# Kernel tuning notes

Measured on AMD Instinct MI355X. Metric: run time of the kernel, lower is better.

Reference implementation:

```python
import jax, jax.numpy as jnp
from jax import lax
import numpy as np

H = 256      # encoder_hidden
F = 256      # variance predictor filter_size
K = 3        # kernel_size
NBINS = 256  # variance_embedding n_bins
B, S, T = 64, 512, 2048


def conv1d(x, w, b, pad):
    # x: [B, L, Cin], w: [K, Cin, Cout] -> [B, L, Cout]
    y = lax.conv_general_dilated(x, w, window_strides=(1,), padding=[(pad, pad)],
                                 dimension_numbers=('NWC', 'WIO', 'NWC'))
    return y + b


def layer_norm(x, g, b, eps=1e-5):
    mu = jnp.mean(x, -1, keepdims=True)
    v = jnp.mean((x - mu) ** 2, -1, keepdims=True)
    return (x - mu) * lax.rsqrt(v + eps) * g + b


def predictor(x, mask, w1, b1, g1, be1, w2, b2, g2, be2, lw, lb):
    h = jax.nn.relu(conv1d(x, w1, b1, (K - 1) // 2))
    h = layer_norm(h, g1, be1)
    h = jax.nn.relu(conv1d(h, w2, b2, 1))  # padding=1 hardcoded in original conv1d_2
    h = layer_norm(h, g2, be2)
    out = (h @ lw + lb)[..., 0]            # [B, L]
    return jnp.where(mask, 0.0, out)       # masked_fill(mask, 0.0)


def setup_inputs():
    key = jax.random.key(0)
    ks = jax.random.split(key, 16)
    inp = {
        'x': jax.random.normal(ks[0], (B, S, H), jnp.float32),
        'pitch_target': jax.random.normal(ks[1], (B, S), jnp.float32),
        'energy_target': jax.random.normal(ks[2], (B, S), jnp.float32),
        'src_mask': jnp.zeros((B, S), bool),
        'duration': jax.random.randint(ks[3], (B, S), 0, 4, jnp.int32),
        'max_len': T,
    }
    i = 4
    for p in ['d', 'p', 'e']:
        inp[p + '_w1'] = jax.random.normal(ks[i], (K, H, F), jnp.float32) * 0.05; i += 1
        inp[p + '_b1'] = jnp.zeros((F,), jnp.float32)
        inp[p + '_g1'] = jnp.ones((F,), jnp.float32)
        inp[p + '_be1'] = jnp.zeros((F,), jnp.float32)
        inp[p + '_w2'] = jax.random.normal(ks[i], (K, F, F), jnp.float32) * 0.05; i += 1
        inp[p + '_b2'] = jnp.zeros((F,), jnp.float32)
        inp[p + '_g2'] = jnp.ones((F,), jnp.float32)
        inp[p + '_be2'] = jnp.zeros((F,), jnp.float32)
        inp[p + '_lw'] = jax.random.normal(ks[i], (F, 1), jnp.float32) * 0.05; i += 1
        inp[p + '_lb'] = jnp.zeros((1,), jnp.float32)
    inp['p_table'] = jax.random.normal(ks[i], (NBINS, H), jnp.float32) * 0.02; i += 1
    inp['e_table'] = jax.random.normal(ks[i], (NBINS, H), jnp.float32) * 0.02
    return inp


def reference(x, pitch_target, energy_target, src_mask, duration, max_len,
              d_w1, d_b1, d_g1, d_be1, d_w2, d_b2, d_g2, d_be2, d_lw, d_lb,
              p_w1, p_b1, p_g1, p_be1, p_w2, p_b2, p_g2, p_be2, p_lw, p_lb,
              e_w1, e_b1, e_g1, e_be1, e_w2, e_b2, e_g2, e_be2, e_lw, e_lb,
              p_table, e_table):
    # linear-quantized bins over the data range (stats.json min/max -> [-2, 2] for randn data)
    bins = jnp.linspace(-2.0, 2.0, NBINS - 1, dtype=jnp.float32)

    log_d_pred = predictor(x, src_mask, d_w1, d_b1, d_g1, d_be1, d_w2, d_b2, d_g2, d_be2, d_lw, d_lb)

    # phoneme-level pitch (training path: target given -> embed bucketized target)
    p_pred = predictor(x, src_mask, p_w1, p_b1, p_g1, p_be1, p_w2, p_b2, p_g2, p_be2, p_lw, p_lb)
    p_emb = p_table[jnp.searchsorted(bins, pitch_target, side='left')]  # torch.bucketize(right=False)
    x = x + p_emb

    # phoneme-level energy (predictor runs on x AFTER pitch embedding, as in original)
    e_pred = predictor(x, src_mask, e_w1, e_b1, e_g1, e_be1, e_w2, e_b2, e_g2, e_be2, e_lw, e_lb)
    e_emb = e_table[jnp.searchsorted(bins, energy_target, side='left')]
    x = x + e_emb

    # Length regulation: expand phoneme i duration[b, i] times, pad to max_len.
    cum = jnp.cumsum(duration, axis=1)                 # [B, S]
    mel_len = cum[:, -1]                               # [B]
    frames = jnp.arange(max_len)                       # [T]
    # frame t maps to first phoneme i with cum[i] > t
    idx = jax.vmap(lambda c: jnp.searchsorted(c, frames, side='right'))(cum)  # [B, T]
    idx = jnp.minimum(idx, duration.shape[1] - 1)
    mel = jnp.take_along_axis(x, idx[:, :, None], axis=1)                     # [B, T, H]
    valid = frames[None, :] < mel_len[:, None]
    mel = jnp.where(valid[:, :, None], mel, 0.0)       # zero-pad beyond mel_len

    d_rounded = duration
    return (mel, p_pred, e_pred, log_d_pred, d_rounded, mel_len)
```

## Files before the change

kernel.cpp:

```cpp
#include <hip/hip_runtime.h>
#include <cstdint>
#include <cstddef>


#define HH 256
#define SS 512
#define BB 64
#define TT 2048

typedef __bf16 bf16;
typedef __attribute__((ext_vector_type(8))) __bf16 bf16x8;
typedef __attribute__((ext_vector_type(4))) __bf16 bf16x4;
typedef __attribute__((ext_vector_type(4))) float f32x4;

static constexpr size_t WSZ  = (size_t)3 * HH * HH;
static constexpr size_t H1SZ = (size_t)BB * SS * HH;

__device__ __forceinline__ int swz(int r, int c) { return (r * HH + c) ^ ((r & 7) << 3); }

__device__ __forceinline__ void gload16(const void* g, void* l) {
    __builtin_amdgcn_global_load_lds(
        (const __attribute__((address_space(1))) unsigned int*)g,
        (__attribute__((address_space(3))) unsigned int*)l, 16, 0, 0);
}

__device__ __forceinline__ float edge_val(int j) {
    const float step = 4.0f / 254.0f;
    if (j == 254) return 2.0f;
    return __fadd_rn(-2.0f, __fmul_rn((float)j, step));
}
__device__ __forceinline__ int bucket256(float v) {
    int lo = 0, hi = 255;
    while (lo < hi) {
        int mid = (lo + hi) >> 1;
        if (edge_val(mid) < v) lo = mid + 1; else hi = mid;
    }
    return lo;
}

__global__ void wt_pack(const float* __restrict__ w0, const float* __restrict__ w1,
                        const float* __restrict__ w2, const float* __restrict__ w3,
                        const float* __restrict__ w4, const float* __restrict__ w5,
                        bf16* __restrict__ wp) {
    const int cv = blockIdx.x / 3, k = blockIdx.x % 3;
    const float* wsel[6] = {w0, w1, w2, w3, w4, w5};
    const float* wk = wsel[cv] + (size_t)k * HH * HH;
    bf16* o = wp + ((size_t)(cv * 3 + k)) * HH * HH;
    for (int fb = 0; fb < 16; ++fb) {
        #pragma unroll
        for (int h = 0; h < 2; ++h) {
            const int idx  = threadIdx.x + 256 * h;
            const int kcb  = idx >> 6, lane = idx & 63;
            const int f    = fb * 16 + (lane & 15);
            const int c0   = kcb * 32 + (lane >> 4) * 8;
            bf16x8 v;
            #pragma unroll
            for (int j = 0; j < 8; ++j) v[j] = (bf16)wk[(size_t)(c0 + j) * HH + f];
            *(bf16x8*)(o + (((size_t)fb * 8 + kcb) * 64 + lane) * 8) = v;
        }
    }
}

__global__ __launch_bounds__(256) void xcvt_kernel(
    const float* __restrict__ x, const float* __restrict__ pt,
    const float* __restrict__ ptab,
    bf16* __restrict__ x1, bf16* __restrict__ x2)
{
    const int row = blockIdx.x * 8 + (threadIdx.x >> 5);
    const int c   = (threadIdx.x & 31) * 8;
    const int pb  = bucket256(pt[row]);
    const float4 v0 = *(const float4*)(x + (size_t)row * HH + c);
    const float4 v1 = *(const float4*)(x + (size_t)row * HH + c + 4);
    const float4 t0 = *(const float4*)(ptab + (size_t)pb * HH + c);
    const float4 t1 = *(const float4*)(ptab + (size_t)pb * HH + c + 4);
    bf16x8 a, b2;
    a[0] = (bf16)v0.x; a[1] = (bf16)v0.y; a[2] = (bf16)v0.z; a[3] = (bf16)v0.w;
    a[4] = (bf16)v1.x; a[5] = (bf16)v1.y; a[6] = (bf16)v1.z; a[7] = (bf16)v1.w;
    b2[0] = (bf16)(v0.x + t0.x); b2[1] = (bf16)(v0.y + t0.y);
    b2[2] = (bf16)(v0.z + t0.z); b2[3] = (bf16)(v0.w + t0.w);
    b2[4] = (bf16)(v1.x + t1.x); b2[5] = (bf16)(v1.y + t1.y);
    b2[6] = (bf16)(v1.z + t1.z); b2[7] = (bf16)(v1.w + t1.w);
    *(bf16x8*)(x1 + (size_t)row * HH + c) = a;
    *(bf16x8*)(x2 + (size_t)row * HH + c) = b2;
}

struct Args3 {
    const float* bias[3];
    const float* g[3];
    const float* be[3];
    const float* lw[3];
    const float* lb[3];
    float*       out[3];
};

__global__ __launch_bounds__(256, 3) void conv_fused(
    const bf16* __restrict__ x1,
    const bf16* __restrict__ x2,
    const bf16* __restrict__ wpk,
    Args3 a1, Args3 a2,
    const uint8_t* __restrict__ mask)
{
    __shared__ alignas(16) bf16 tile[84 * HH];
    __shared__ float red_s[80][4], red_q[80][4];
    __shared__ float ln_m[80], ln_r[80];

    const int tid    = threadIdx.x;
    const int pred   = blockIdx.x >> 9;
    const int within = blockIdx.x & 511;
    const int b      = within >> 3;
    const int s0     = (within & 7) * 64;

    const int lane = tid & 63;
    const int wv   = tid >> 6;

    const bf16* inb = (pred == 2 ? x2 : x1) + (size_t)b * SS * HH;
    const bf16* wt1 = wpk + (size_t)(pred * 2) * WSZ;
    const bf16* wt2 = wt1 + WSZ;

    for (int c = wv; c < 42; c += 4) {
        const int rrow = 2 * c + (lane >> 5);
        const int s    = s0 - 9 + rrow;
        const int sc   = min(max(s, 0), SS - 1);
        const char* src = (const char*)inb + (size_t)sc * 512
                        + (((lane & 31) * 16) ^ ((rrow & 7) << 4));
        gload16(src, (char*)tile + (size_t)c * 1024);
    }
    __syncthreads();
    if (s0 == 0) {
        for (int idx = tid; idx < 9 * 32; idx += 256) {
            const int r = idx >> 5, o = idx & 31;
            ((uint4*)tile)[r * 32 + o] = make_uint4(0u, 0u, 0u, 0u);
        }
    }
    if (s0 == SS - 64) {
        for (int idx = tid; idx < 11 * 32; idx += 256) {
            const int r = 73 + (idx >> 5), o = idx & 31;
            ((uint4*)tile)[r * 32 + o] = make_uint4(0u, 0u, 0u, 0u);
        }
    }
    __syncthreads();

    const int ln15 = lane & 15;
    const int g8   = (lane >> 4) << 3;
    const int q4   = (lane >> 4) << 2;

    f32x4 acc1[4][5];
    #pragma unroll
    for (int mf = 0; mf < 4; ++mf)
        #pragma unroll
        for (int sf = 0; sf < 5; ++sf) acc1[mf][sf] = f32x4{0.f, 0.f, 0.f, 0.f};

    #pragma unroll 2
    for (int t = 0; t < 24; ++t) {
        const int k = t >> 3, kcb = t & 7;
        const int kc = kcb << 5;
        bf16x8 aw[4], bx[5];
        const bf16* bp = wt1 + ((((size_t)k * 16 + wv * 4) * 8 + kcb) << 9)
                       + (size_t)lane * 8;
        #pragma unroll
        for (int mf = 0; mf < 4; ++mf)
            aw[mf] = *(const bf16x8*)(bp + ((size_t)mf << 12));
        #pragma unroll
        for (int sf = 0; sf < 5; ++sf)
            bx[sf] = *(const bf16x8*)&tile[swz(16 * sf + ln15 + k, kc + g8)];
        #pragma unroll
        for (int mf = 0; mf < 4; ++mf)
            #pragma unroll
            for (int sf = 0; sf < 5; ++sf)
                acc1[mf][sf] = __builtin_amdgcn_mfma_f32_16x16x32_bf16(
                    aw[mf], bx[sf], acc1[mf][sf], 0, 0, 0);
    }

    #pragma unroll
    for (int mf = 0; mf < 4; ++mf)
        #pragma unroll
        for (int i = 0; i < 4; ++i) {
            const float bv = a1.bias[pred][64 * wv + 16 * mf + q4 + i];
            #pragma unroll
            for (int sf = 0; sf < 5; ++sf)
                acc1[mf][sf][i] = fmaxf(acc1[mf][sf][i] + bv, 0.f);
        }

    #pragma unroll
    for (int sf = 0; sf < 5; ++sf) {
        float s = 0.f, q = 0.f;
        #pragma unroll
        for (int mf = 0; mf < 4; ++mf)
            #pragma unroll
            for (int i = 0; i < 4; ++i) {
                const float v = acc1[mf][sf][i];
                s += v; q += v * v;
            }
        s += __shfl_xor(s, 16); s += __shfl_xor(s, 32);
        q += __shfl_xor(q, 16); q += __shfl_xor(q, 32);
        if (lane < 16) { red_s[16 * sf + lane][wv] = s; red_q[16 * sf + lane][wv] = q; }
    }
    __syncthreads();
    if (tid < 80) {
        const float s = red_s[tid][0] + red_s[tid][1] + red_s[tid][2] + red_s[tid][3];
        const float q = red_q[tid][0] + red_q[tid][1] + red_q[tid][2] + red_q[tid][3];
        const float mean = s * (1.f / 256.f);
        const float var  = q * (1.f / 256.f) - mean * mean;
        ln_m[tid] = mean;
        ln_r[tid] = rsqrtf(var + 1e-5f);
    }
    __syncthreads();

    {
        float g1v[4][4], be1v[4][4];
        #pragma unroll
        for (int mf = 0; mf < 4; ++mf)
            #pragma unroll
            for (int i = 0; i < 4; ++i) {
                const int f1 = 64 * wv + 16 * mf + q4 + i;
                g1v[mf][i]  = a1.g[pred][f1];
                be1v[mf][i] = a1.be[pred][f1];
            }
        #pragma unroll
        for (int sf = 0; sf < 5; ++sf) {
            const int o  = 16 * sf + ln15;
            const int hr = o - 7;
            const float mean = ln_m[o], rs = ln_r[o];
            const bool ok = (o >= 7 && o <= 72);
            #pragma unroll
            for (int mf = 0; mf < 4; ++mf) {
                bf16x4 hv;
                #pragma unroll
                for (int i = 0; i < 4; ++i)
                    hv[i] = (bf16)((acc1[mf][sf][i] - mean) * rs * g1v[mf][i] + be1v[mf][i]);
                if (ok)
                    *(bf16x4*)&tile[swz(hr, 64 * wv + 16 * mf + q4)] = hv;
            }
        }
    }
    __syncthreads();
    if (tid < 64) {
        if (s0 == 0)       *(uint2*)&tile[tid * 4]           = make_uint2(0u, 0u);
        if (s0 == SS - 64) *(uint2*)&tile[65 * HH + tid * 4] = make_uint2(0u, 0u);
    }
    __syncthreads();

    f32x4 acc2[4][4];
    #pragma unroll
    for (int mf = 0; mf < 4; ++mf)
        #pragma unroll
        for (int sf = 0; sf < 4; ++sf) acc2[mf][sf] = f32x4{0.f, 0.f, 0.f, 0.f};

    #pragma unroll 2
    for (int t = 0; t < 24; ++t) {
        const int k = t >> 3, kcb = t & 7;
        const int kc = kcb << 5;
        bf16x8 aw[4], bx[4];
        const bf16* bp = wt2 + ((((size_t)k * 16 + wv * 4) * 8 + kcb) << 9)
                       + (size_t)lane * 8;
        #pragma unroll
        for (int mf = 0; mf < 4; ++mf)
            aw[mf] = *(const bf16x8*)(bp + ((size_t)mf << 12));
        #pragma unroll
        for (int sf = 0; sf < 4; ++sf)
            bx[sf] = *(const bf16x8*)&tile[swz(16 * sf + ln15 + k, kc + g8)];
        #pragma unroll
        for (int mf = 0; mf < 4; ++mf)
            #pragma unroll
            for (int sf = 0; sf < 4; ++sf)
                acc2[mf][sf] = __builtin_amdgcn_mfma_f32_16x16x32_bf16(
                    aw[mf], bx[sf], acc2[mf][sf], 0, 0, 0);
    }

    #pragma unroll
    for (int mf = 0; mf < 4; ++mf)
        #pragma unroll
        for (int i = 0; i < 4; ++i) {
            const float bv = a2.bias[pred][64 * wv + 16 * mf + q4 + i];
            #pragma unroll
            for (int sf = 0; sf < 4; ++sf)
                acc2[mf][sf][i] = fmaxf(acc2[mf][sf][i] + bv, 0.f);
        }

    #pragma unroll
    for (int sf = 0; sf < 4; ++sf) {
        float s = 0.f, q = 0.f;
        #pragma unroll
        for (int mf = 0; mf < 4; ++mf)
            #pragma unroll
            for (int i = 0; i < 4; ++i) {
                const float v = acc2[mf][sf][i];
                s += v; q += v * v;
            }
        s += __shfl_xor(s, 16); s += __shfl_xor(s, 32);
        q += __shfl_xor(q, 16); q += __shfl_xor(q, 32);
        if (lane < 16) { red_s[16 * sf + lane][wv] = s; red_q[16 * sf + lane][wv] = q; }
    }
    __syncthreads();
    if (tid < 64) {
        const float s = red_s[tid][0] + red_s[tid][1] + red_s[tid][2] + red_s[tid][3];
        const float q = red_q[tid][0] + red_q[tid][1] + red_q[tid][2] + red_q[tid][3];
        const float mean = s * (1.f / 256.f);
        const float var  = q * (1.f / 256.f) - mean * mean;
        ln_m[tid] = mean;
        ln_r[tid] = rsqrtf(var + 1e-5f);
    }
    __syncthreads();

    {
        float c1v[4][4], cbv[4][4];
        #pragma unroll
        for (int mf = 0; mf < 4; ++mf)
            #pragma unroll
            for (int i = 0; i < 4; ++i) {
                const int f2 = 64 * wv + 16 * mf + q4 + i;
                const float lwv = a2.lw[pred][f2];
                c1v[mf][i] = a2.g[pred][f2] * lwv;
                cbv[mf][i] = a2.be[pred][f2] * lwv;
            }
        #pragma unroll
        for (int sf = 0; sf < 4; ++sf) {
            const int so = 16 * sf + ln15;
            const float mean = ln_m[so], rs = ln_r[so];
            float t = 0.f;
            #pragma unroll
            for (int mf = 0; mf < 4; ++mf)
                #pragma unroll
                for (int i = 0; i < 4; ++i)
                    t += (acc2[mf][sf][i] - mean) * rs * c1v[mf][i] + cbv[mf][i];
            t += __shfl_xor(t, 16); t += __shfl_xor(t, 32);
            if (lane < 16) red_s[16 * sf + lane][wv] = t;
        }
        __syncthreads();
        if (tid < 64) {
            const int gr = b * SS + s0 + tid;
            const float dv = red_s[tid][0] + red_s[tid][1] + red_s[tid][2] + red_s[tid][3]
                           + a2.lb[pred][0];
            a2.out[pred][gr] = mask[gr] ? 0.f : dv;
        }
    }
}

__global__ void dur_kernel(const int* __restrict__ dur, int* __restrict__ idxb,
                           int* __restrict__ mli,
                           float* __restrict__ drnd, float* __restrict__ mlen) {
    __shared__ int sb[SS];
    const int b = blockIdx.x, t = threadIdx.x;
    const int v = dur[b * SS + t];
    drnd[b * SS + t] = (float)v;
    sb[t] = v;
    __syncthreads();
    for (int off = 1; off < SS; off <<= 1) {
        const int add = (t >= off) ? sb[t - off] : 0;
        __syncthreads();
        sb[t] += add;
        __syncthreads();
    }
    const int hi = sb[t];
    const int lo = hi - v;
    for (int j = lo; j < hi; ++j) idxb[b * TT + j] = t;
    if (t == SS - 1) { mlen[b] = (float)hi; mli[b] = hi; }
}

__global__ __launch_bounds__(256) void gather_kernel(
    const float* __restrict__ x,
    const float* __restrict__ ptab, const float* __restrict__ pt,
    const float* __restrict__ etab, const float* __restrict__ et,
    const int* __restrict__ idxb, const int* __restrict__ mli,
    float* __restrict__ mel)
{
    const int lane = threadIdx.x & 63;
    for (int row = blockIdx.x * 4 + (threadIdx.x >> 6); row < BB * TT; row += 4096 * 4) {
        const int b = row >> 11;
        const int t = row & (TT - 1);
        float4 v = make_float4(0.f, 0.f, 0.f, 0.f);
        if (t < mli[b]) {
            const int idx = idxb[row];
            const size_t src = ((size_t)b * SS + idx) * HH + lane * 4;
            v = *(const float4*)(x + src);
            const int pb = bucket256(pt[b * SS + idx]);
            const int eb = bucket256(et[b * SS + idx]);
            const float4 pv = *(const float4*)(ptab + (size_t)pb * HH + lane * 4);
            const float4 ev = *(const float4*)(etab + (size_t)eb * HH + lane * 4);
            v.x += pv.x + ev.x; v.y += pv.y + ev.y; v.z += pv.z + ev.z; v.w += pv.w + ev.w;
        }
        *(float4*)(mel + (size_t)row * HH + lane * 4) = v;
    }
}

extern "C" void kernel_launch(void* const* d_in, const int* in_sizes, int n_in,
                              void* d_out, int out_size, void* d_ws, size_t ws_size,
                              hipStream_t stream) {
    (void)in_sizes; (void)n_in; (void)out_size; (void)ws_size;

    const float*   x      = (const float*)d_in[0];
    const float*   pitch  = (const float*)d_in[1];
    const float*   energy = (const float*)d_in[2];
    const uint8_t* mask   = (const uint8_t*)d_in[3];
    const int*     dur    = (const int*)d_in[4];
    const float*   ptab   = (const float*)d_in[36];
    const float*   etab   = (const float*)d_in[37];

    float* out = (float*)d_out;
    const size_t N_MEL = (size_t)BB * TT * HH;
    float* out_p  = out + N_MEL;
    float* out_e  = out_p + (size_t)BB * SS;
    float* out_ld = out_e + (size_t)BB * SS;
    float* out_dr = out_ld + (size_t)BB * SS;
    float* out_ml = out_dr + (size_t)BB * SS;

    bf16* wpk  = (bf16*)d_ws;
    int*  idxb = (int*)(wpk + 6 * WSZ);
    int*  mli  = idxb + (size_t)BB * TT;

    bf16* x1 = (bf16*)out;
    bf16* x2 = x1 + H1SZ;

    wt_pack<<<18, 256, 0, stream>>>(
        (const float*)d_in[6],  (const float*)d_in[10],
        (const float*)d_in[16], (const float*)d_in[20],
        (const float*)d_in[26], (const float*)d_in[30],
        wpk);
    xcvt_kernel<<<(BB * SS) / 8, 256, 0, stream>>>(x, pitch, ptab, x1, x2);
    dur_kernel<<<BB, SS, 0, stream>>>(dur, idxb, mli, out_dr, out_ml);

    Args3 a1 = {
        {(const float*)d_in[7],  (const float*)d_in[17], (const float*)d_in[27]},
        {(const float*)d_in[8],  (const float*)d_in[18], (const float*)d_in[28]},
        {(const float*)d_in[9],  (const float*)d_in[19], (const float*)d_in[29]},
        {nullptr, nullptr, nullptr}, {nullptr, nullptr, nullptr},
        {nullptr, nullptr, nullptr}
    };
    Args3 a2 = {
        {(const float*)d_in[11], (const float*)d_in[21], (const float*)d_in[31]},
        {(const float*)d_in[12], (const float*)d_in[22], (const float*)d_in[32]},
        {(const float*)d_in[13], (const float*)d_in[23], (const float*)d_in[33]},
        {(const float*)d_in[14], (const float*)d_in[24], (const float*)d_in[34]},
        {(const float*)d_in[15], (const float*)d_in[25], (const float*)d_in[35]},
        {out_ld, out_p, out_e}
    };

    conv_fused<<<3 * 512, 256, 0, stream>>>(x1, x2, wpk, a1, a2, mask);

    gather_kernel<<<4096, 256, 0, stream>>>(x, ptab, pitch, etab, energy, idxb, mli, out);
}
```

Before: 152.1 us.

## Replace XOR-swizzled LDS tile with padded stride and register-staged loads

Switches the shared-memory activation tile from an XOR-swizzled 256-wide layout filled by direct global-to-LDS loads to a padded row stride of 264 elements, filled through ordinary vector loads with in-loop zeroing of out-of-range rows. It also seeds the MFMA accumulators with the bias instead of adding the bias after the GEMM. The padding is meant to avoid LDS bank conflicts with simpler address arithmetic. In exchange it drops the asynchronous global_load_lds path, stages the data through registers, and uses slightly more LDS per block, which could affect occupancy.

Measured after the change: 151.0 us. About the same (-0.7%).

```diff
diff --git a/kernel.cpp b/kernel.cpp
--- a/kernel.cpp
+++ b/kernel.cpp
@@ -7,6 +7,7 @@
 #define SS 512
 #define BB 64
 #define TT 2048
+#define LSTR 264
 
 typedef __bf16 bf16;
 typedef __attribute__((ext_vector_type(8))) __bf16 bf16x8;
@@ -15,14 +16,6 @@
 
 static constexpr size_t WSZ  = (size_t)3 * HH * HH;
 static constexpr size_t H1SZ = (size_t)BB * SS * HH;
-
-__device__ __forceinline__ int swz(int r, int c) { return (r * HH + c) ^ ((r & 7) << 3); }
-
-__device__ __forceinline__ void gload16(const void* g, void* l) {
-    __builtin_amdgcn_global_load_lds(
-        (const __attribute__((address_space(1))) unsigned int*)g,
-        (__attribute__((address_space(3))) unsigned int*)l, 16, 0, 0);
-}
 
 __device__ __forceinline__ float edge_val(int j) {
     const float step = 4.0f / 254.0f;
@@ -100,7 +93,7 @@
     Args3 a1, Args3 a2,
     const uint8_t* __restrict__ mask)
 {
-    __shared__ alignas(16) bf16 tile[84 * HH];
+    __shared__ alignas(16) bf16 tile[82 * LSTR];
     __shared__ float red_s[80][4], red_q[80][4];
     __shared__ float ln_m[80], ln_r[80];
 
@@ -117,26 +110,13 @@
     const bf16* wt1 = wpk + (size_t)(pred * 2) * WSZ;
     const bf16* wt2 = wt1 + WSZ;
 
-    for (int c = wv; c < 42; c += 4) {
-        const int rrow = 2 * c + (lane >> 5);
-        const int s    = s0 - 9 + rrow;
-        const int sc   = min(max(s, 0), SS - 1);
-        const char* src = (const char*)inb + (size_t)sc * 512
-                        + (((lane & 31) * 16) ^ ((rrow & 7) << 4));
-        gload16(src, (char*)tile + (size_t)c * 1024);
-    }
-    __syncthreads();
-    if (s0 == 0) {
-        for (int idx = tid; idx < 9 * 32; idx += 256) {
-            const int r = idx >> 5, o = idx & 31;
-            ((uint4*)tile)[r * 32 + o] = make_uint4(0u, 0u, 0u, 0u);
-        }
-    }
-    if (s0 == SS - 64) {
-        for (int idx = tid; idx < 11 * 32; idx += 256) {
-            const int r = 73 + (idx >> 5), o = idx & 31;
-            ((uint4*)tile)[r * 32 + o] = make_uint4(0u, 0u, 0u, 0u);
-        }
+    for (int idx = tid; idx < 82 * 32; idx += 256) {
+        const int r   = idx >> 5, c16 = idx & 31;
+        const int s   = s0 - 9 + r;
+        bf16x8 v = {};
+        if (s >= 0 && s < SS)
+            v = *(const bf16x8*)(inb + (size_t)s * HH + c16 * 8);
+        *(bf16x8*)&tile[r * LSTR + c16 * 8] = v;
     }
     __syncthreads();
 
@@ -144,11 +124,18 @@
     const int g8   = (lane >> 4) << 3;
     const int q4   = (lane >> 4) << 2;
 
+    f32x4 bini[4];
+    #pragma unroll
+    for (int mf = 0; mf < 4; ++mf)
+        #pragma unroll
+        for (int i = 0; i < 4; ++i)
+            bini[mf][i] = a1.bias[pred][64 * wv + 16 * mf + q4 + i];
+
     f32x4 acc1[4][5];
     #pragma unroll
     for (int mf = 0; mf < 4; ++mf)
         #pragma unroll
-        for (int sf = 0; sf < 5; ++sf) acc1[mf][sf] = f32x4{0.f, 0.f, 0.f, 0.f};
+        for (int sf = 0; sf < 5; ++sf) acc1[mf][sf] = bini[mf];
 
     #pragma unroll 2
     for (int t = 0; t < 24; ++t) {
@@ -162,7 +149,7 @@
             aw[mf] = *(const bf16x8*)(bp + ((size_t)mf << 12));
         #pragma unroll
         for (int sf = 0; sf < 5; ++sf)
-            bx[sf] = *(const bf16x8*)&tile[swz(16 * sf + ln15 + k, kc + g8)];
+            bx[sf] = *(const bf16x8*)&tile[(16 * sf + ln15 + k) * LSTR + kc + g8];
         #pragma unroll
         for (int mf = 0; mf < 4; ++mf)
             #pragma unroll
@@ -174,12 +161,10 @@
     #pragma unroll
     for (int mf = 0; mf < 4; ++mf)
         #pragma unroll
-        for (int i = 0; i < 4; ++i) {
-            const float bv = a1.bias[pred][64 * wv + 16 * mf + q4 + i];
-            #pragma unroll
-            for (int sf = 0; sf < 5; ++sf)
-                acc1[mf][sf][i] = fmaxf(acc1[mf][sf][i] + bv, 0.f);
-        }
+        for (int sf = 0; sf < 5; ++sf)
+            #pragma unroll
+            for (int i = 0; i < 4; ++i)
+                acc1[mf][sf][i] = fmaxf(acc1[mf][sf][i], 0.f);
 
     #pragma unroll
     for (int sf = 0; sf < 5; ++sf) {
@@ -229,22 +214,28 @@
                 for (int i = 0; i < 4; ++i)
                     hv[i] = (bf16)((acc1[mf][sf][i] - mean) * rs * g1v[mf][i] + be1v[mf][i]);
                 if (ok)
-                    *(bf16x4*)&tile[swz(hr, 64 * wv + 16 * mf + q4)] = hv;
+                    *(bf16x4*)&tile[hr * LSTR + 64 * wv + 16 * mf + q4] = hv;
             }
         }
     }
     __syncthreads();
     if (tid < 64) {
-        if (s0 == 0)       *(uint2*)&tile[tid * 4]           = make_uint2(0u, 0u);
-        if (s0 == SS - 64) *(uint2*)&tile[65 * HH + tid * 4] = make_uint2(0u, 0u);
-    }
-    __syncthreads();
+        if (s0 == 0)       *(uint2*)&tile[tid * 4]            = make_uint2(0u, 0u);
+        if (s0 == SS - 64) *(uint2*)&tile[65 * LSTR + tid * 4] = make_uint2(0u, 0u);
+    }
+    __syncthreads();
+
+    #pragma unroll
+    for (int mf = 0; mf < 4; ++mf)
+        #pragma unroll
+        for (int i = 0; i < 4; ++i)
+            bini[mf][i] = a2.bias[pred][64 * wv + 16 * mf + q4 + i];
 
     f32x4 acc2[4][4];
     #pragma unroll
     for (int mf = 0; mf < 4; ++mf)
         #pragma unroll
-        for (int sf = 0; sf < 4; ++sf) acc2[mf][sf] = f32x4{0.f, 0.f, 0.f, 0.f};
+        for (int sf = 0; sf < 4; ++sf) acc2[mf][sf] = bini[mf];
 
     #pragma unroll 2
     for (int t = 0; t < 24; ++t) {
@@ -258,7 +249,7 @@
             aw[mf] = *(const bf16x8*)(bp + ((size_t)mf << 12));
         #pragma unroll
         for (int sf = 0; sf < 4; ++sf)
-            bx[sf] = *(const bf16x8*)&tile[swz(16 * sf + ln15 + k, kc + g8)];
+            bx[sf] = *(const bf16x8*)&tile[(16 * sf + ln15 + k) * LSTR + kc + g8];
         #pragma unroll
         for (int mf = 0; mf < 4; ++mf)
             #pragma unroll
@@ -270,12 +261,10 @@
     #pragma unroll
     for (int mf = 0; mf < 4; ++mf)
         #pragma unroll
-        for (int i = 0; i < 4; ++i) {
-            const float bv = a2.bias[pred][64 * wv + 16 * mf + q4 + i];
-            #pragma unroll
-            for (int sf = 0; sf < 4; ++sf)
-                acc2[mf][sf][i] = fmaxf(acc2[mf][sf][i] + bv, 0.f);
-        }
+        for (int sf = 0; sf < 4; ++sf)
+            #pragma unroll
+            for (int i = 0; i < 4; ++i)
+                acc2[mf][sf][i] = fmaxf(acc2[mf][sf][i], 0.f);
 
     #pragma unroll
     for (int sf = 0; sf < 4; ++sf) {
```
